# Kernel optimization log

Measured on AMD Instinct MI355X. Metric: run time of the kernel, lower is better.

Reference implementation:

```python
import jax, jax.numpy as jnp
import numpy as np

EMB = 1024
N_HEADS = 16
HEAD = EMB // N_HEADS
EPS = 1e-5


def layernorm(x, g, b):
    mu = jnp.mean(x, axis=-1, keepdims=True)
    var = jnp.var(x, axis=-1, keepdims=True)
    return (x - mu) * jax.lax.rsqrt(var + EPS) * g + b


def setup_inputs() -> dict:
    key = jax.random.key(0)
    ks = jax.random.split(key, 12)
    s = lambda fan_in: 1.0 / np.sqrt(fan_in)
    return {
        "x": jax.random.normal(ks[0], (8, 1024, EMB), dtype=jnp.float32),
        "ln1_g": jnp.ones((EMB,), jnp.float32),
        "ln1_b": jnp.zeros((EMB,), jnp.float32),
        "wq": jax.random.uniform(ks[1], (EMB, EMB), jnp.float32, -s(EMB), s(EMB)),
        "wk": jax.random.uniform(ks[2], (EMB, EMB), jnp.float32, -s(EMB), s(EMB)),
        "wv": jax.random.uniform(ks[3], (EMB, EMB), jnp.float32, -s(EMB), s(EMB)),
        "w_proj": jax.random.uniform(ks[4], (EMB, EMB), jnp.float32, -s(EMB), s(EMB)),
        "b_proj": jnp.zeros((EMB,), jnp.float32),
        "ln2_g": jnp.ones((EMB,), jnp.float32),
        "ln2_b": jnp.zeros((EMB,), jnp.float32),
        "w1": jax.random.uniform(ks[5], (EMB, 4 * EMB), jnp.float32, -s(EMB), s(EMB)),
        "b1": jnp.zeros((4 * EMB,), jnp.float32),
        "w2": jax.random.uniform(ks[6], (4 * EMB, EMB), jnp.float32, -s(4 * EMB), s(4 * EMB)),
        "b2": jnp.zeros((EMB,), jnp.float32),
    }


def reference(x, ln1_g, ln1_b, wq, wk, wv, w_proj, b_proj, ln2_g, ln2_b, w1, b1, w2, b2):
    B, T, E = x.shape
    h = layernorm(x, ln1_g, ln1_b)
    # per-head no-bias projections == one big matmul then split into heads
    q = (h @ wq).reshape(B, T, N_HEADS, HEAD).transpose(0, 2, 1, 3)  # [B,H,T,D]
    k = (h @ wk).reshape(B, T, N_HEADS, HEAD).transpose(0, 2, 1, 3)
    v = (h @ wv).reshape(B, T, N_HEADS, HEAD).transpose(0, 2, 1, 3)
    scores = jnp.einsum("bhqd,bhkd->bhqk", q, k) * (HEAD ** -0.5)
    causal = jnp.tril(jnp.ones((T, T), dtype=bool))
    scores = jnp.where(causal, scores, -jnp.inf)
    wei = jax.nn.softmax(scores, axis=-1)  # dropout is identity at eval
    attn = jnp.einsum("bhqk,bhkd->bhqd", wei, v)
    attn = attn.transpose(0, 2, 1, 3).reshape(B, T, E)
    out = x + attn @ w_proj + b_proj
    h2 = layernorm(out, ln2_g, ln2_b)
    mlp = jax.nn.gelu(h2 @ w1 + b1, approximate=False) @ w2 + b2
    return out + mlp
```

## Files before the change

### kernel.cpp

```cpp
#include <hip/hip_runtime.h>
#include <hip/hip_bf16.h>

#define EMB 1024
#define NH 16
#define HD 64
#define BATCH 8
#define SEQ 1024
#define ROWS (BATCH*SEQ)

typedef unsigned short ushort_t;
typedef __attribute__((ext_vector_type(8))) short bf16x8;
typedef __attribute__((ext_vector_type(4))) float f32x4;
typedef __attribute__((ext_vector_type(16))) float f32x16;

__device__ __forceinline__ float bf2f(ushort_t u){
    union { unsigned int i; float f; } v; v.i = ((unsigned int)u) << 16; return v.f;
}
__device__ __forceinline__ ushort_t f2bf(float f){
    unsigned int u = __float_as_uint(f);
    unsigned int r = (u + 0x7FFFu + ((u >> 16) & 1u)) >> 16;
    return (ushort_t)r;
}
__device__ __forceinline__ void gload16(const ushort_t* g, ushort_t* l){
    __builtin_amdgcn_global_load_lds(
        (const __attribute__((address_space(1))) void*)g,
        (__attribute__((address_space(3))) void*)l,
        16, 0, 0);
}
__device__ __forceinline__ float gelu_f(float v){
    float x = fabsf(v) * 0.70710678118654752f;
    float t = __builtin_amdgcn_rcpf(1.0f + 0.3275911f * x);
    float poly = t*(0.254829592f + t*(-0.284496736f + t*(1.421413741f + t*(-1.453152027f + t*1.061405429f))));
    float erfa = 1.0f - poly * __expf(-x*x);
    float erfv = (v >= 0.f) ? erfa : -erfa;
    return 0.5f * v * (1.0f + erfv);
}

__global__ __launch_bounds__(256) void prep_kernel(const float* __restrict__ x,
                                                   const float* __restrict__ ln1_g,
                                                   const float* __restrict__ ln1_b,
                                                   ushort_t* __restrict__ h1,
                                                   const float* __restrict__ wq,
                                                   const float* __restrict__ wk,
                                                   const float* __restrict__ wv,
                                                   const float* __restrict__ w_proj,
                                                   const float* __restrict__ w1,
                                                   const float* __restrict__ w2,
                                                   ushort_t* __restrict__ wqkv_t,
                                                   ushort_t* __restrict__ wproj_t,
                                                   ushort_t* __restrict__ w1_t,
                                                   ushort_t* __restrict__ w2_t){
    int bid = blockIdx.x;
    int tid = threadIdx.x;
    if (bid < ROWS){
        __shared__ float ss[4], qq[4];
        __shared__ float mu_s, sc_s;
        const float* xr = x + (size_t)bid * EMB;
        float4 f = *(const float4*)(xr + tid*4);
        float v[4] = {f.x, f.y, f.z, f.w};
        float s = v[0]+v[1]+v[2]+v[3];
        float q = v[0]*v[0]+v[1]*v[1]+v[2]*v[2]+v[3]*v[3];
        #pragma unroll
        for (int o = 32; o > 0; o >>= 1){ s += __shfl_down(s, o); q += __shfl_down(q, o); }
        int wave = tid >> 6, lane = tid & 63;
        if (lane == 0){ ss[wave] = s; qq[wave] = q; }
        __syncthreads();
        if (tid == 0){
            float S = ss[0]+ss[1]+ss[2]+ss[3];
            float Q = qq[0]+qq[1]+qq[2]+qq[3];
            float mu = S * (1.0f/EMB);
            float var = Q * (1.0f/EMB) - mu*mu;
            mu_s = mu; sc_s = rsqrtf(var + 1e-5f);
        }
        __syncthreads();
        float mu = mu_s, sc = sc_s;
        float4 gu = *(const float4*)(ln1_g + tid*4);
        float4 bu = *(const float4*)(ln1_b + tid*4);
        ushort4 o4;
        o4.x = f2bf((v[0]-mu)*sc*gu.x + bu.x);
        o4.y = f2bf((v[1]-mu)*sc*gu.y + bu.y);
        o4.z = f2bf((v[2]-mu)*sc*gu.z + bu.z);
        o4.w = f2bf((v[3]-mu)*sc*gu.w + bu.w);
        *(ushort4*)(h1 + (size_t)bid*EMB + tid*4) = o4;
    } else {
        __shared__ ushort_t t[32][33];
        int j = bid - ROWS;
        const float* in; ushort_t* out; int K, N, bx, by;
        if (j < 3072){
            int which = j >> 10, jj = j & 1023;
            in = (which == 0) ? wq : (which == 1) ? wk : wv;
            out = wqkv_t + (size_t)which * 1024 * 1024;
            K = 1024; N = 1024; bx = jj & 31; by = jj >> 5;
        } else if (j < 4096){
            int jj = j - 3072;
            in = w_proj; out = wproj_t; K = 1024; N = 1024; bx = jj & 31; by = jj >> 5;
        } else if (j < 8192){
            int jj = j - 4096;
            in = w1; out = w1_t; K = 1024; N = 4096; bx = jj & 127; by = jj >> 7;
        } else {
            int jj = j - 8192;
            in = w2; out = w2_t; K = 4096; N = 1024; bx = jj & 31; by = jj >> 5;
        }
        int tx = tid & 31, ty = tid >> 5;
        #pragma unroll
        for (int r = 0; r < 4; ++r)
            t[ty + r*8][tx] = f2bf(in[(size_t)(by*32 + ty + r*8) * N + bx*32 + tx]);
        __syncthreads();
        #pragma unroll
        for (int r = 0; r < 4; ++r)
            out[(size_t)(bx*32 + ty + r*8) * K + by*32 + tx] = t[tx][ty + r*8];
    }
}

__global__ __launch_bounds__(256) void ln_kernel(const float* __restrict__ xin,
                                                 const float* __restrict__ g,
                                                 const float* __restrict__ bia,
                                                 ushort_t* __restrict__ out){
    int row = blockIdx.x;
    int tid = threadIdx.x;
    const float* x = xin + (size_t)row * EMB;
    float4 f = *(const float4*)(x + tid*4);
    float v[4] = {f.x, f.y, f.z, f.w};
    float s = v[0]+v[1]+v[2]+v[3];
    float q = v[0]*v[0]+v[1]*v[1]+v[2]*v[2]+v[3]*v[3];
    #pragma unroll
    for (int o = 32; o > 0; o >>= 1){ s += __shfl_down(s, o); q += __shfl_down(q, o); }
    __shared__ float ss[4], qq[4];
    __shared__ float mu_s, sc_s;
    int wave = tid >> 6, lane = tid & 63;
    if (lane == 0){ ss[wave] = s; qq[wave] = q; }
    __syncthreads();
    if (tid == 0){
        float S = ss[0]+ss[1]+ss[2]+ss[3];
        float Q = qq[0]+qq[1]+qq[2]+qq[3];
        float mu = S * (1.0f/EMB);
        float var = Q * (1.0f/EMB) - mu*mu;
        mu_s = mu; sc_s = rsqrtf(var + 1e-5f);
    }
    __syncthreads();
    float mu = mu_s, sc = sc_s;
    float4 gu = *(const float4*)(g + tid*4);
    float4 bu = *(const float4*)(bia + tid*4);
    ushort4 o4;
    o4.x = f2bf((v[0]-mu)*sc*gu.x + bu.x);
    o4.y = f2bf((v[1]-mu)*sc*gu.y + bu.y);
    o4.z = f2bf((v[2]-mu)*sc*gu.z + bu.z);
    o4.w = f2bf((v[3]-mu)*sc*gu.w + bu.w);
    *(ushort4*)(out + (size_t)row*EMB + tid*4) = o4;
}

template<int MODE>
__global__ __launch_bounds__(512, 4) void gemm_kernel(const ushort_t* __restrict__ A,
                                                      const ushort_t* __restrict__ Bt,
                                                      const float* __restrict__ bias,
                                                      const float* __restrict__ resid,
                                                      void* __restrict__ out,
                                                      int M, int N, int K){
    __shared__ ushort_t As[2][128*64];
    __shared__ ushort_t Bs[2][128*64];
    int tid = threadIdx.x;
    int lane = tid & 63, wave = tid >> 6;
    int l31 = lane & 31, half = lane >> 5;
    int wm = wave >> 1, wn = wave & 1;
    int bid = blockIdx.x;
    int m0 = (bid & 63) * 128, n0 = (bid >> 6) * 128;

    f32x16 acc[2];
    #pragma unroll
    for (int j=0;j<2;j++)
        #pragma unroll
        for (int r=0;r<16;r++) acc[j][r] = 0.f;

    int lr  = lane >> 3;
    int lch = lane & 7;
    const ushort_t* gA = A  + (size_t)(m0 + wave*16 + lr)*K + (lch ^ lr)*8;
    const ushort_t* gB = Bt + (size_t)(n0 + wave*16 + lr)*K + (lch ^ lr)*8;
    int lo = (wave*16)*64;
    int sx = lane & 7;
    int NT = K >> 6;

#define GTILE(B, T)                                                                       \
    {                                                                                     \
        if ((T) + 1 < NT){                                                                \
            int nk0 = ((T) + 1) << 6;                                                     \
            gload16(gA + nk0,               &As[(B)^1][lo]);                              \
            gload16(gA + (size_t)8*K + nk0, &As[(B)^1][lo + 8*64]);                       \
            gload16(gB + nk0,               &Bs[(B)^1][lo]);                              \
            gload16(gB + (size_t)8*K + nk0, &Bs[(B)^1][lo + 8*64]);                       \
            asm volatile("s_waitcnt vmcnt(4)" ::: "memory");                              \
        } else {                                                                          \
            asm volatile("s_waitcnt vmcnt(0)" ::: "memory");                              \
        }                                                                                 \
        __builtin_amdgcn_s_barrier();                                                     \
        asm volatile("" ::: "memory");                                                    \
        _Pragma("unroll")                                                                 \
        for (int s = 0; s < 4; ++s){                                                      \
            int ch = ((s<<1) | half) ^ sx;                                                \
            bf16x8 af  = *(const bf16x8*)&As[B][(wm*32 + l31)*64 + ch*8];                 \
            bf16x8 bf0 = *(const bf16x8*)&Bs[B][(wn*64 + l31)*64 + ch*8];                 \
            bf16x8 bf1 = *(const bf16x8*)&Bs[B][(wn*64 + 32 + l31)*64 + ch*8];            \
            acc[0] = __builtin_amdgcn_mfma_f32_32x32x16_bf16(af, bf0, acc[0], 0,0,0);     \
            acc[1] = __builtin_amdgcn_mfma_f32_32x32x16_bf16(af, bf1, acc[1], 0,0,0);     \
        }                                                                                 \
        asm volatile("" ::: "memory");                                                    \
        __builtin_amdgcn_s_barrier();                                                     \
        asm volatile("" ::: "memory");                                                    \
    }

    gload16(gA,               &As[0][lo]);
    gload16(gA + (size_t)8*K, &As[0][lo + 8*64]);
    gload16(gB,               &Bs[0][lo]);
    gload16(gB + (size_t)8*K, &Bs[0][lo + 8*64]);

    for (int t = 0; t < NT; t += 2){
        GTILE(0, t)
        GTILE(1, t+1)
    }
#undef GTILE

    int rowoff = 4*half;
    #pragma unroll
    for (int j=0;j<2;j++){
        int n = n0 + wn*64 + j*32 + l31;
        #pragma unroll
        for (int reg=0; reg<16; ++reg){
            int m = m0 + wm*32 + (reg&3) + 8*(reg>>2) + rowoff;
            float v = acc[j][reg];
            size_t idx = (size_t)m*N + n;
            if (MODE == 0){
                ((ushort_t*)out)[idx] = f2bf(v);
            } else if (MODE == 1){
                v += bias[n] + resid[idx];
                ((float*)out)[idx] = v;
            } else if (MODE == 2){
                v += bias[n];
                ((ushort_t*)out)[idx] = f2bf(gelu_f(v));
            } else {
                v += bias[n] + resid[idx];
                ((float*)out)[idx] = v;
            }
        }
    }
}

__global__ __launch_bounds__(256) void attn_kernel(const ushort_t* __restrict__ qkv,
                                                   ushort_t* __restrict__ attn_out){
    __shared__ ushort_t Qs[128*64];
    __shared__ ushort_t Ks[64*64];
    __shared__ ushort_t Vts[64][72];
    __shared__ ushort_t Ps[128*64];

    int tid = threadIdx.x;
    int lane = tid & 63, wave = tid >> 6;
    int quad = lane >> 4, l15 = lane & 15;
    int pair = blockIdx.x;
    int bh = blockIdx.y;
    int b = bh >> 4, h = bh & 15;
    size_t tb = (size_t)b * SEQ;

    int lr = lane >> 3, lch = lane & 7;
    int tr = tid >> 3;
    int tc = (tid & 7) * 8;
    int sw_w = tid & 7;
    int sx = l15 & 7;

    for (int t = 0; t < 2; ++t){
        int qi = t ? (7 - pair) : pair;

        {
            const ushort_t* gq = qkv + (size_t)(tb + qi*128 + wave*32 + lr)*3072 + h*64 + (lch^lr)*8;
            ushort_t* lq = &Qs[(wave*32)*64];
            #pragma unroll
            for (int p = 0; p < 4; ++p)
                gload16(gq + (size_t)(p*8)*3072, lq + p*8*64);
        }

        f32x4 o_acc[4][2];
        #pragma unroll
        for (int i=0;i<4;i++)
            #pragma unroll
            for (int j=0;j<2;j++) o_acc[i][j] = (f32x4){0.f,0.f,0.f,0.f};
        float m_st[2] = {-1e30f, -1e30f};
        float l_st[2] = {0.f, 0.f};

        int nj = 2*qi + 2;
        for (int j = 0; j < nj; ++j){
            {
                const ushort_t* gk = qkv + (size_t)(tb + j*64 + wave*16 + lr)*3072 + 1024 + h*64 + (lch^lr)*8;
                ushort_t* lk = &Ks[(wave*16)*64];
                gload16(gk, lk);
                gload16(gk + (size_t)8*3072, lk + 8*64);
            }
            #pragma unroll
            for (int p = 0; p < 2; ++p){
                int r = tr + p*32;
                bf16x8 vv = *(const bf16x8*)(qkv + (size_t)(tb + j*64 + r)*3072 + 2048 + h*64 + tc);
                int kcol = r ^ (sw_w << 3);
                #pragma unroll
                for (int c = 0; c < 8; ++c) Vts[tc + c][kcol] = (ushort_t)vv[c];
            }
            __syncthreads();

            f32x4 st[4][2];
            #pragma unroll
            for (int mt=0;mt<4;mt++)
                #pragma unroll
                for (int nt=0;nt<2;nt++) st[mt][nt] = (f32x4){0.f,0.f,0.f,0.f};
            #pragma unroll
            for (int kf = 0; kf < 2; ++kf){
                int ch = (kf*4 + quad) ^ sx;
                bf16x8 ak[4], bq[2];
                #pragma unroll
                for (int mt=0;mt<4;mt++) ak[mt] = *(const bf16x8*)&Ks[(mt*16 + l15)*64 + ch*8];
                #pragma unroll
                for (int nt=0;nt<2;nt++) bq[nt] = *(const bf16x8*)&Qs[(wave*32 + nt*16 + l15)*64 + ch*8];
                #pragma unroll
                for (int mt=0;mt<4;mt++)
                    #pragma unroll
                    for (int nt=0;nt<2;nt++)
                        st[mt][nt] = __builtin_amdgcn_mfma_f32_16x16x32_bf16(ak[mt], bq[nt], st[mt][nt], 0,0,0);
            }

            bool need_mask = (j >= 2*qi);
            #pragma unroll
            for (int mt=0;mt<4;mt++)
                #pragma unroll
                for (int nt=0;nt<2;nt++)
                    #pragma unroll
                    for (int r=0;r<4;r++){
                        float s = st[mt][nt][r] * 0.125f;
                        if (need_mask){
                            int kg = j*64 + mt*16 + quad*4 + r;
                            int qg = qi*128 + wave*32 + nt*16 + l15;
                            if (kg > qg) s = -1e30f;
                        }
                        st[mt][nt][r] = s;
                    }

            #pragma unroll
            for (int nt = 0; nt < 2; ++nt){
                float mx = st[0][nt][0];
                #pragma unroll
                for (int mt=0;mt<4;mt++)
                    #pragma unroll
                    for (int r=0;r<4;r++) mx = fmaxf(mx, st[mt][nt][r]);
                mx = fmaxf(mx, __shfl_xor(mx, 16));
                mx = fmaxf(mx, __shfl_xor(mx, 32));
                float mnew = fmaxf(m_st[nt], mx);
                float al = __expf(m_st[nt] - mnew);
                float ps = 0.f;
                #pragma unroll
                for (int mt=0;mt<4;mt++)
                    #pragma unroll
                    for (int r=0;r<4;r++){
                        float p = __expf(st[mt][nt][r] - mnew);
                        st[mt][nt][r] = p;
                        ps += p;
                    }
                ps += __shfl_xor(ps, 16);
                ps += __shfl_xor(ps, 32);
                l_st[nt] = l_st[nt]*al + ps;
                m_st[nt] = mnew;
                #pragma unroll
                for (int mtd=0;mtd<4;mtd++)
                    #pragma unroll
                    for (int r=0;r<4;r++) o_acc[mtd][nt][r] *= al;
                #pragma unroll
                for (int mt=0;mt<4;mt++){
                    int slot = (mt*2 + (quad>>1)) ^ sx;
                    ushort4 pk;
                    pk.x = f2bf(st[mt][nt][0]); pk.y = f2bf(st[mt][nt][1]);
                    pk.z = f2bf(st[mt][nt][2]); pk.w = f2bf(st[mt][nt][3]);
                    *(ushort4*)&Ps[(wave*32 + nt*16 + l15)*64 + slot*8 + (quad&1)*4] = pk;
                }
            }

            #pragma unroll
            for (int kf = 0; kf < 2; ++kf){
                bf16x8 av[4], bp[2];
                #pragma unroll
                for (int mtd=0;mtd<4;mtd++){
                    int d = mtd*16 + l15;
                    int col = (kf*32 + quad*8) ^ (((d >> 3) & 7) << 3);
                    av[mtd] = *(const bf16x8*)&Vts[d][col];
                }
                #pragma unroll
                for (int nt=0;nt<2;nt++){
                    int ch = (kf*4 + quad) ^ sx;
                    bp[nt] = *(const bf16x8*)&Ps[(wave*32 + nt*16 + l15)*64 + ch*8];
                }
                #pragma unroll
                for (int mtd=0;mtd<4;mtd++)
                    #pragma unroll
                    for (int nt=0;nt<2;nt++)
                        o_acc[mtd][nt] = __builtin_amdgcn_mfma_f32_16x16x32_bf16(av[mtd], bp[nt], o_acc[mtd][nt], 0,0,0);
            }
            __syncthreads();
        }

        #pragma unroll
        for (int nt = 0; nt < 2; ++nt){
            float inv = 1.0f / l_st[nt];
            size_t tok = tb + qi*128 + wave*32 + nt*16 + l15;
            #pragma unroll
            for (int mtd = 0; mtd < 4; ++mtd){
                ushort4 ok;
                ok.x = f2bf(o_acc[mtd][nt][0]*inv); ok.y = f2bf(o_acc[mtd][nt][1]*inv);
                ok.z = f2bf(o_acc[mtd][nt][2]*inv); ok.w = f2bf(o_acc[mtd][nt][3]*inv);
                *(ushort4*)(attn_out + tok*EMB + h*64 + mtd*16 + quad*4) = ok;
            }
        }
    }
}

extern "C" void kernel_launch(void* const* d_in, const int* in_sizes, int n_in,
                              void* d_out, int out_size, void* d_ws, size_t ws_size,
                              hipStream_t stream){
    const float* x      = (const float*)d_in[0];
    const float* ln1_g  = (const float*)d_in[1];
    const float* ln1_b  = (const float*)d_in[2];
    const float* wq     = (const float*)d_in[3];
    const float* wk     = (const float*)d_in[4];
    const float* wv     = (const float*)d_in[5];
    const float* w_proj = (const float*)d_in[6];
    const float* b_proj = (const float*)d_in[7];
    const float* ln2_g  = (const float*)d_in[8];
    const float* ln2_b  = (const float*)d_in[9];
    const float* w1     = (const float*)d_in[10];
    const float* b1     = (const float*)d_in[11];
    const float* w2     = (const float*)d_in[12];
    const float* b2     = (const float*)d_in[13];
    float* outp = (float*)d_out;

    char* ws = (char*)d_ws;
    size_t off = 0;
    auto alloc = [&](size_t bytes)->char*{ char* p = ws + off; off += (bytes + 255) & ~255ULL; return p; };
    ushort_t* wqkv_t = (ushort_t*)alloc((size_t)3072*1024*2);
    ushort_t* wproj_t= (ushort_t*)alloc((size_t)1024*1024*2);
    ushort_t* w1_t   = (ushort_t*)alloc((size_t)4096*1024*2);
    ushort_t* w2_t   = (ushort_t*)alloc((size_t)1024*4096*2);
    ushort_t* qkv    = (ushort_t*)alloc((size_t)ROWS*3072*2);
    ushort_t* hbuf   = (ushort_t*)alloc((size_t)ROWS*1024*2);
    float*    out32  = (float*)  alloc((size_t)ROWS*1024*4);
    ushort_t* mid    = (ushort_t*)alloc((size_t)ROWS*4096*2);
    ushort_t* h1 = hbuf;
    ushort_t* attn = hbuf;
    ushort_t* h2 = qkv;

    dim3 blk(256);
    dim3 gblk(512);
    prep_kernel<<<dim3(20480), blk, 0, stream>>>(x, ln1_g, ln1_b, h1,
                                                 wq, wk, wv, w_proj, w1, w2,
                                                 wqkv_t, wproj_t, w1_t, w2_t);
    gemm_kernel<0><<<dim3(64*(3072/128)), gblk, 0, stream>>>(h1, wqkv_t, nullptr, nullptr, qkv, ROWS, 3072, 1024);
    attn_kernel<<<dim3(4,128), blk, 0, stream>>>(qkv, attn);
    gemm_kernel<1><<<dim3(64*(1024/128)), gblk, 0, stream>>>(attn, wproj_t, b_proj, x, out32, ROWS, 1024, 1024);
    ln_kernel<<<ROWS, blk, 0, stream>>>(out32, ln2_g, ln2_b, h2);
    gemm_kernel<2><<<dim3(64*(4096/128)), gblk, 0, stream>>>(h2, w1_t, b1, nullptr, mid, ROWS, 4096, 1024);
    gemm_kernel<3><<<dim3(64*(1024/128)), gblk, 0, stream>>>(mid, w2_t, b2, out32, outp, ROWS, 1024, 4096);
}
```

Before: 458.3 us.

## Split GEMM K-tile across wave groups with 64x64 warp tiles and LDS reduction

Restructures the GEMM so each of 4 wave pairs computes a 64x64 output subtile (2x2 MFMA blocks), with two wave groups splitting each 64-wide K tile. Partial sums are reduced through LDS at the end. LDS now holds the MFMA fragment layout directly instead of a swizzled row layout. The aim is more register reuse per LDS read and fewer bank conflicts. The cost is doubled accumulator registers, an extra reduction pass and barrier, and only half the waves doing the epilogue.

```diff
diff --git a/kernel.cpp b/kernel.cpp
--- a/kernel.cpp
+++ b/kernel.cpp
@@ -156,37 +156,45 @@
                                                       const float* __restrict__ resid,
                                                       void* __restrict__ out,
                                                       int M, int N, int K){
-    __shared__ ushort_t As[2][128*64];
-    __shared__ ushort_t Bs[2][128*64];
+    __shared__ ushort_t S[32768];
+    ushort_t* const As0 = S;
+    ushort_t* const As1 = S + 8192;
+    ushort_t* const Bs0 = S + 16384;
+    ushort_t* const Bs1 = S + 24576;
+
     int tid = threadIdx.x;
-    int lane = tid & 63, wave = tid >> 6;
+    int lane = tid & 63, w = tid >> 6;
     int l31 = lane & 31, half = lane >> 5;
-    int wm = wave >> 1, wn = wave & 1;
+    int kg = w >> 2, w2 = w & 3;
+    int wm = w2 >> 1, wn = w2 & 1;
     int bid = blockIdx.x;
     int m0 = (bid & 63) * 128, n0 = (bid >> 6) * 128;
 
-    f32x16 acc[2];
+    f32x16 acc[2][2];
     #pragma unroll
-    for (int j=0;j<2;j++)
-        #pragma unroll
-        for (int r=0;r<16;r++) acc[j][r] = 0.f;
-
-    int lr  = lane >> 3;
-    int lch = lane & 7;
-    const ushort_t* gA = A  + (size_t)(m0 + wave*16 + lr)*K + (lch ^ lr)*8;
-    const ushort_t* gB = Bt + (size_t)(n0 + wave*16 + lr)*K + (lch ^ lr)*8;
-    int lo = (wave*16)*64;
-    int sx = lane & 7;
+    for (int i=0;i<2;i++)
+        #pragma unroll
+        for (int j=0;j<2;j++)
+            #pragma unroll
+            for (int r=0;r<16;r++) acc[i][j][r] = 0.f;
+
+    const ushort_t* gA0 = A  + (size_t)(m0 + (w>>2)*32 + l31)*K + (w&3)*16 + half*8;
+    const ushort_t* gA1 = gA0 + (size_t)64*K;
+    const ushort_t* gB0 = Bt + (size_t)(n0 + (w>>2)*32 + l31)*K + (w&3)*16 + half*8;
+    const ushort_t* gB1 = gB0 + (size_t)64*K;
     int NT = K >> 6;
 
-#define GTILE(B, T)                                                                       \
+#define STAGE(AD, BD, k0s)                                                                \
+    gload16(gA0 + (k0s), &AD[w*512]);                                                     \
+    gload16(gA1 + (k0s), &AD[(w+8)*512]);                                                 \
+    gload16(gB0 + (k0s), &BD[w*512]);                                                     \
+    gload16(gB1 + (k0s), &BD[(w+8)*512]);
+
+#define GTILE(AC, BC, AN, BN, T)                                                          \
     {                                                                                     \
         if ((T) + 1 < NT){                                                                \
             int nk0 = ((T) + 1) << 6;                                                     \
-            gload16(gA + nk0,               &As[(B)^1][lo]);                              \
-            gload16(gA + (size_t)8*K + nk0, &As[(B)^1][lo + 8*64]);                       \
-            gload16(gB + nk0,               &Bs[(B)^1][lo]);                              \
-            gload16(gB + (size_t)8*K + nk0, &Bs[(B)^1][lo + 8*64]);                       \
+            STAGE(AN, BN, nk0)                                                            \
             asm volatile("s_waitcnt vmcnt(4)" ::: "memory");                              \
         } else {                                                                          \
             asm volatile("s_waitcnt vmcnt(0)" ::: "memory");                              \
@@ -194,50 +202,83 @@
         __builtin_amdgcn_s_barrier();                                                     \
         asm volatile("" ::: "memory");                                                    \
         _Pragma("unroll")                                                                 \
-        for (int s = 0; s < 4; ++s){                                                      \
-            int ch = ((s<<1) | half) ^ sx;                                                \
-            bf16x8 af  = *(const bf16x8*)&As[B][(wm*32 + l31)*64 + ch*8];                 \
-            bf16x8 bf0 = *(const bf16x8*)&Bs[B][(wn*64 + l31)*64 + ch*8];                 \
-            bf16x8 bf1 = *(const bf16x8*)&Bs[B][(wn*64 + 32 + l31)*64 + ch*8];            \
-            acc[0] = __builtin_amdgcn_mfma_f32_32x32x16_bf16(af, bf0, acc[0], 0,0,0);     \
-            acc[1] = __builtin_amdgcn_mfma_f32_32x32x16_bf16(af, bf1, acc[1], 0,0,0);     \
+        for (int s2 = 0; s2 < 2; ++s2){                                                   \
+            int s = kg*2 + s2;                                                            \
+            bf16x8 af[2], bf[2];                                                          \
+            _Pragma("unroll")                                                             \
+            for (int i=0;i<2;i++) af[i] = *(const bf16x8*)&AC[((wm*2+i)*4 + s)*512 + lane*8]; \
+            _Pragma("unroll")                                                             \
+            for (int j=0;j<2;j++) bf[j] = *(const bf16x8*)&BC[((wn*2+j)*4 + s)*512 + lane*8]; \
+            _Pragma("unroll")                                                             \
+            for (int i=0;i<2;i++)                                                         \
+                _Pragma("unroll")                                                         \
+                for (int j=0;j<2;j++)                                                     \
+                    acc[i][j] = __builtin_amdgcn_mfma_f32_32x32x16_bf16(af[i], bf[j], acc[i][j], 0,0,0); \
         }                                                                                 \
         asm volatile("" ::: "memory");                                                    \
         __builtin_amdgcn_s_barrier();                                                     \
         asm volatile("" ::: "memory");                                                    \
     }
 
-    gload16(gA,               &As[0][lo]);
-    gload16(gA + (size_t)8*K, &As[0][lo + 8*64]);
-    gload16(gB,               &Bs[0][lo]);
-    gload16(gB + (size_t)8*K, &Bs[0][lo + 8*64]);
+    STAGE(As0, Bs0, 0)
 
     for (int t = 0; t < NT; t += 2){
-        GTILE(0, t)
-        GTILE(1, t+1)
+        GTILE(As0, Bs0, As1, Bs1, t)
+        GTILE(As1, Bs1, As0, Bs0, t+1)
     }
 #undef GTILE
-
-    int rowoff = 4*half;
-    #pragma unroll
-    for (int j=0;j<2;j++){
-        int n = n0 + wn*64 + j*32 + l31;
-        #pragma unroll
-        for (int reg=0; reg<16; ++reg){
-            int m = m0 + wm*32 + (reg&3) + 8*(reg>>2) + rowoff;
-            float v = acc[j][reg];
-            size_t idx = (size_t)m*N + n;
-            if (MODE == 0){
-                ((ushort_t*)out)[idx] = f2bf(v);
-            } else if (MODE == 1){
-                v += bias[n] + resid[idx];
-                ((float*)out)[idx] = v;
-            } else if (MODE == 2){
-                v += bias[n];
-                ((ushort_t*)out)[idx] = f2bf(gelu_f(v));
-            } else {
-                v += bias[n] + resid[idx];
-                ((float*)out)[idx] = v;
+#undef STAGE
+
+    float* red = (float*)S;
+    if (kg == 1){
+        float* rbase = red + w2*4096;
+        #pragma unroll
+        for (int i=0;i<2;i++)
+            #pragma unroll
+            for (int j=0;j<2;j++)
+                #pragma unroll
+                for (int rq=0;rq<4;rq++){
+                    f32x4 v = { acc[i][j][rq*4], acc[i][j][rq*4+1], acc[i][j][rq*4+2], acc[i][j][rq*4+3] };
+                    *(f32x4*)&rbase[(i*2+j)*1024 + rq*256 + lane*4] = v;
+                }
+    }
+    __syncthreads();
+    if (kg == 0){
+        float* rbase = red + w2*4096;
+        #pragma unroll
+        for (int i=0;i<2;i++)
+            #pragma unroll
+            for (int j=0;j<2;j++)
+                #pragma unroll
+                for (int rq=0;rq<4;rq++){
+                    f32x4 p = *(const f32x4*)&rbase[(i*2+j)*1024 + rq*256 + lane*4];
+                    #pragma unroll
+                    for (int c=0;c<4;c++) acc[i][j][rq*4+c] += p[c];
+                }
+        int rowoff = 4*half;
+        #pragma unroll
+        for (int i=0;i<2;i++){
+            #pragma unroll
+            for (int j=0;j<2;j++){
+                int n = n0 + wn*64 + j*32 + l31;
+                #pragma unroll
+                for (int reg=0; reg<16; ++reg){
+                    int m = m0 + wm*64 + i*32 + (reg&3) + 8*(reg>>2) + rowoff;
+                    float v = acc[i][j][reg];
+                    size_t idx = (size_t)m*N + n;
+                    if (MODE == 0){
+                        ((ushort_t*)out)[idx] = f2bf(v);
+                    } else if (MODE == 1){
+                        v += bias[n] + resid[idx];
+                        ((float*)out)[idx] = v;
+                    } else if (MODE == 2){
+                        v += bias[n];
+                        ((ushort_t*)out)[idx] = f2bf(gelu_f(v));
+                    } else {
+                        v += bias[n] + resid[idx];
+                        ((float*)out)[idx] = v;
+                    }
+                }
             }
         }
     }
```

Result: slower. 580.2 us (+26.6%).
